# Performance work log

Measured on AMD Instinct MI355X. Metric: run time of the kernel, lower is better.

The kernel has to match this reference:

```python
import jax, jax.numpy as jnp
import numpy as np
import math

SIZE = 1024

def setup_inputs() -> dict:
    key = jax.random.key(0)
    k1, k2, k3, k4, k5 = jax.random.split(key, 5)
    B, Lq, Lc, D = 16, 2048, 2048, SIZE
    query = jax.random.normal(k1, (B, Lq, D), dtype=jnp.float32)
    bank = jax.random.normal(k2, (B, Lc, D), dtype=jnp.float32)
    # Linear weights stored torch-style as [out, in]; scaled like default init
    s = 1.0 / math.sqrt(D)
    Wc = jax.random.normal(k3, (D, D), dtype=jnp.float32) * s
    Woq = jax.random.normal(k4, (D, D), dtype=jnp.float32) * s
    Woc = jax.random.normal(k5, (D, D), dtype=jnp.float32) * s
    return {"query": query, "bank": bank, "Wc": Wc, "Woq": Woq, "Woc": Woc}

def reference(query, bank, Wc, Woq, Woc):
    # general attention: score = q @ (Wc bank)^T / sqrt(d)
    d = query.shape[-1]
    ctx_proj = jnp.einsum('bkd,ed->bke', bank, Wc)          # fc_context(bank)
    score = jnp.einsum('bqd,bkd->bqk', query, ctx_proj) / jnp.sqrt(jnp.float32(d))
    attn = jax.nn.softmax(score, axis=-1)                    # [B, Lq, Lc]
    context = jnp.einsum('bqk,bkd->bqd', attn, bank)
    output = jnp.einsum('bqd,ed->bqe', context, Woc) + jnp.einsum('bqd,ed->bqe', query, Woq)
    return (output, attn)
```

## Files before the change

### kernel.cpp

```cpp
#include <hip/hip_runtime.h>
#include <cstdint>

typedef unsigned short u16;
typedef __attribute__((ext_vector_type(8))) __bf16 bf16x8;
typedef __attribute__((ext_vector_type(4))) float f32x4;
typedef __attribute__((ext_vector_type(4))) unsigned short u16x4;

__device__ __forceinline__ u16 f2bf(float f) {
  unsigned u = __float_as_uint(f);
  u += 0x7fff + ((u >> 16) & 1);
  return (u16)(u >> 16);
}

__device__ __forceinline__ void g2l16(const void* g, void* l) {
  __builtin_amdgcn_global_load_lds(
      (const __attribute__((address_space(1))) unsigned int*)g,
      (__attribute__((address_space(3))) unsigned int*)l, 16, 0, 0);
}

template <int OUT_BF16>
__global__ void gemm_nt(const u16* __restrict__ A, const u16* __restrict__ B,
                        void* __restrict__ Cv,
                        int lda, int ldb, int ldc,
                        long sA, long sB, long sC,
                        int K, float scale)
{
  __shared__ char sm[16384];
  char* As = sm;
  char* Bs = sm + 8192;
  const int t = threadIdx.x;
  const int z = blockIdx.z;
  const u16* Ab = A + (long)z * sA + (long)(blockIdx.y * 128) * lda;
  const u16* Bb = B + (long)z * sB + (long)(blockIdx.x * 128) * ldb;

  const int wave = t >> 6, lane = t & 63;
  const int lm = lane & 15, quad = lane >> 4;
  const int wm = (wave >> 1) * 64, wn = (wave & 1) * 64;

  f32x4 acc[4][4] = {};

  const int sr = t >> 2;
  const int sc = (t & 3) * 8;
  const long aoff0 = (long)sr * lda + sc;
  const long aoff1 = (long)(sr + 64) * lda + sc;
  const long boff0 = (long)sr * ldb + sc;
  const long boff1 = (long)(sr + 64) * ldb + sc;
  char* lA0 = As + t * 16;  char* lA1 = As + 4096 + t * 16;
  char* lB0 = Bs + t * 16;  char* lB1 = Bs + 4096 + t * 16;

  for (int k0 = 0; k0 < K; k0 += 32) {
    __syncthreads();
    g2l16(Ab + aoff0 + k0, lA0);
    g2l16(Ab + aoff1 + k0, lA1);
    g2l16(Bb + boff0 + k0, lB0);
    g2l16(Bb + boff1 + k0, lB1);
    __syncthreads();

    bf16x8 af[4], bg[4];
#pragma unroll
    for (int i = 0; i < 4; ++i) {
      af[i] = *(const bf16x8*)(As + ((wm + i * 16 + lm) * 32 + quad * 8) * 2);
      bg[i] = *(const bf16x8*)(Bs + ((wn + i * 16 + lm) * 32 + quad * 8) * 2);
    }
#pragma unroll
    for (int i = 0; i < 4; ++i)
#pragma unroll
      for (int j = 0; j < 4; ++j)
        acc[i][j] = __builtin_amdgcn_mfma_f32_16x16x32_bf16(af[i], bg[j], acc[i][j], 0, 0, 0);
  }

  const int row0 = blockIdx.y * 128 + wm + quad * 4;
  const int col0 = blockIdx.x * 128 + wn + lm;
  if (OUT_BF16) {
    u16* C = (u16*)Cv + (long)z * sC;
#pragma unroll
    for (int i = 0; i < 4; ++i)
#pragma unroll
      for (int j = 0; j < 4; ++j)
#pragma unroll
        for (int r = 0; r < 4; ++r)
          C[(long)(row0 + i * 16 + r) * ldc + (col0 + j * 16)] = f2bf(acc[i][j][r] * scale);
  } else {
    float* C = (float*)Cv + (long)z * sC;
#pragma unroll
    for (int i = 0; i < 4; ++i)
#pragma unroll
      for (int j = 0; j < 4; ++j)
#pragma unroll
        for (int r = 0; r < 4; ++r)
          C[(long)(row0 + i * 16 + r) * ldc + (col0 + j * 16)] = acc[i][j][r] * scale;
  }
}

__global__ void softmax_rows(float* __restrict__ S, u16* __restrict__ P)
{
  const long row = blockIdx.x;
  float* p = S + row * 2048;
  u16*  q = P + row * 2048;
  const int t = threadIdx.x;
  float4 v0 = ((const float4*)p)[t];
  float4 v1 = ((const float4*)p)[t + 256];

  float m = fmaxf(fmaxf(fmaxf(v0.x, v0.y), fmaxf(v0.z, v0.w)),
                  fmaxf(fmaxf(v1.x, v1.y), fmaxf(v1.z, v1.w)));
#pragma unroll
  for (int s = 32; s; s >>= 1) m = fmaxf(m, __shfl_xor(m, s));
  __shared__ float red[4];
  if ((t & 63) == 0) red[t >> 6] = m;
  __syncthreads();
  m = fmaxf(fmaxf(red[0], red[1]), fmaxf(red[2], red[3]));

  v0.x = __expf(v0.x - m); v0.y = __expf(v0.y - m);
  v0.z = __expf(v0.z - m); v0.w = __expf(v0.w - m);
  v1.x = __expf(v1.x - m); v1.y = __expf(v1.y - m);
  v1.z = __expf(v1.z - m); v1.w = __expf(v1.w - m);

  float s8 = ((v0.x + v0.y) + (v0.z + v0.w)) + ((v1.x + v1.y) + (v1.z + v1.w));
#pragma unroll
  for (int s = 32; s; s >>= 1) s8 += __shfl_xor(s8, s);
  __syncthreads();
  if ((t & 63) == 0) red[t >> 6] = s8;
  __syncthreads();
  s8 = red[0] + red[1] + red[2] + red[3];
  const float inv = 1.0f / s8;

  v0.x *= inv; v0.y *= inv; v0.z *= inv; v0.w *= inv;
  v1.x *= inv; v1.y *= inv; v1.z *= inv; v1.w *= inv;
  ((float4*)p)[t] = v0;
  ((float4*)p)[t + 256] = v1;
  u16x4 b0 = { f2bf(v0.x), f2bf(v0.y), f2bf(v0.z), f2bf(v0.w) };
  u16x4 b1 = { f2bf(v1.x), f2bf(v1.y), f2bf(v1.z), f2bf(v1.w) };
  ((u16x4*)q)[t] = b0;
  ((u16x4*)q)[t + 256] = b1;
}

__global__ void transpose_cvt(const float* __restrict__ in, u16* __restrict__ out)
{
  __shared__ float tile[32][33];
  const int z = blockIdx.z;
  const float* ib = in + (long)z * 2048 * 1024;
  u16* ob = out + (long)z * 1024 * 2048;
  const int c0 = blockIdx.x * 32, r0 = blockIdx.y * 32;
  const int tx = threadIdx.x, ty = threadIdx.y;
#pragma unroll
  for (int k = 0; k < 32; k += 8)
    tile[ty + k][tx] = ib[(long)(r0 + ty + k) * 1024 + c0 + tx];
  __syncthreads();
#pragma unroll
  for (int k = 0; k < 32; k += 8)
    ob[(long)(c0 + ty + k) * 2048 + r0 + tx] = f2bf(tile[tx][ty + k]);
}

__global__ void cvt_bf16(const float* __restrict__ in, u16* __restrict__ out,
                         int ldo, long n)
{
  long i = ((long)blockIdx.x * 256 + threadIdx.x) * 4;
  if (i >= n) return;
  float4 v = *(const float4*)(in + i);
  long row = i >> 10;
  int col = (int)(i & 1023);
  u16x4 b = { f2bf(v.x), f2bf(v.y), f2bf(v.z), f2bf(v.w) };
  *(u16x4*)(out + row * (long)ldo + col) = b;
}

extern "C" void kernel_launch(void* const* d_in, const int* in_sizes, int n_in,
                              void* d_out, int out_size, void* d_ws, size_t ws_size,
                              hipStream_t stream)
{
  (void)in_sizes; (void)n_in; (void)out_size; (void)ws_size;
  const float* query = (const float*)d_in[0];
  const float* bank  = (const float*)d_in[1];
  const float* Wc    = (const float*)d_in[2];
  const float* Woq   = (const float*)d_in[3];
  const float* Woc   = (const float*)d_in[4];

  const long B = 16, L = 2048, D = 1024;
  float* out  = (float*)d_out;
  float* attn = out + B * L * D;

  u16* kb   = (u16*)d_ws;
  u16* cpb  = kb + B * L * D;
  u16* ab   = kb;
  u16* kbT  = cpb + B * L * D;
  u16* Acat = kbT + B * D * L;
  u16* Wcb  = Acat + B * L * 2048;
  u16* Wcat = Wcb + D * D;

  const long nQ = B * L * D;
  const long nW = D * D;

  cvt_bf16<<<dim3((unsigned)(nQ / 4 / 256)), 256, 0, stream>>>(bank, kb, 1024, nQ);
  cvt_bf16<<<dim3((unsigned)(nQ / 4 / 256)), 256, 0, stream>>>(query, Acat + 1024, 2048, nQ);
  cvt_bf16<<<dim3((unsigned)(nW / 4 / 256)), 256, 0, stream>>>(Wc, Wcb, 1024, nW);
  cvt_bf16<<<dim3((unsigned)(nW / 4 / 256)), 256, 0, stream>>>(Woc, Wcat, 2048, nW);
  cvt_bf16<<<dim3((unsigned)(nW / 4 / 256)), 256, 0, stream>>>(Woq, Wcat + 1024, 2048, nW);
  transpose_cvt<<<dim3(32, 64, 16), dim3(32, 8), 0, stream>>>(bank, kbT);

  gemm_nt<1><<<dim3(8, 16, 16), 256, 0, stream>>>(kb, Wcb, cpb,
      1024, 1024, 1024, L * D, 0, L * D, 1024, 1.0f);
  gemm_nt<0><<<dim3(16, 16, 16), 256, 0, stream>>>(Acat + 1024, cpb, attn,
      2048, 1024, 2048, L * 2048, L * D, L * 2048, 1024, 0.03125f);
  softmax_rows<<<dim3((unsigned)(B * L)), 256, 0, stream>>>(attn, ab);
  gemm_nt<1><<<dim3(8, 16, 16), 256, 0, stream>>>(ab, kbT, Acat,
      2048, 2048, 2048, L * 2048, D * 2048, L * 2048, 2048, 1.0f);
  gemm_nt<0><<<dim3(8, 16, 16), 256, 0, stream>>>(Acat, Wcat, out,
      2048, 2048, 1024, L * 2048, 0, L * D, 2048, 1.0f);
}
```

Baseline: 1.352 ms.

## Replace GEMM with 256x256 tiled, 4-stage LDS-pipelined 8-wave kernel

Replaces the single-buffered 128x128 GEMM with a 256x256-tile, 512-thread kernel. It uses a 4-deep ring of LDS buffers (128 KB dynamic shared memory) filled by async global-to-LDS loads, XOR-swizzled LDS addressing to avoid bank conflicts, and explicit vmcnt/barrier scheduling so loads overlap MFMA work. Block IDs are remapped for L2 locality, and MFMA sections raise wave priority. The aim is to remove the per-iteration load stalls and low arithmetic intensity of the old kernel. In exchange it uses much more LDS, which limits occupancy, and launches fewer blocks per GEMM.

```diff
diff --git a/kernel.cpp b/kernel.cpp
--- a/kernel.cpp
+++ b/kernel.cpp
@@ -18,63 +18,118 @@
       (__attribute__((address_space(3))) unsigned int*)l, 16, 0, 0);
 }
 
+__device__ __forceinline__ int swz(int q) { return q ^ (((q >> 7) & 7) << 4); }
+
 template <int OUT_BF16>
-__global__ void gemm_nt(const u16* __restrict__ A, const u16* __restrict__ B,
-                        void* __restrict__ Cv,
-                        int lda, int ldb, int ldc,
-                        long sA, long sB, long sC,
-                        int K, float scale)
-{
-  __shared__ char sm[16384];
-  char* As = sm;
-  char* Bs = sm + 8192;
+__global__ __launch_bounds__(512, 2)
+void gemm_nt_8p(const u16* __restrict__ A, const u16* __restrict__ B,
+                void* __restrict__ Cv,
+                int lda, int ldb, int ldc,
+                long sA, long sB, long sC,
+                int K, float scale)
+{
+  extern __shared__ char sm[];
   const int t = threadIdx.x;
+  const int lane = t & 63, wave = t >> 6;
+  const int lm = lane & 15, quad = lane >> 4;
+  const int wr = wave >> 2, wc = wave & 3;
+
+  const int gx = (int)gridDim.x;
+  const int npz = gx * (int)gridDim.y;
+  int lid = (int)blockIdx.x + gx * (int)blockIdx.y;
+  lid = (lid & 7) * (npz >> 3) + (lid >> 3);
+  const int bx = lid % gx, by = lid / gx;
   const int z = blockIdx.z;
-  const u16* Ab = A + (long)z * sA + (long)(blockIdx.y * 128) * lda;
-  const u16* Bb = B + (long)z * sB + (long)(blockIdx.x * 128) * ldb;
-
-  const int wave = t >> 6, lane = t & 63;
-  const int lm = lane & 15, quad = lane >> 4;
-  const int wm = (wave >> 1) * 64, wn = (wave & 1) * 64;
-
-  f32x4 acc[4][4] = {};
-
-  const int sr = t >> 2;
-  const int sc = (t & 3) * 8;
-  const long aoff0 = (long)sr * lda + sc;
-  const long aoff1 = (long)(sr + 64) * lda + sc;
-  const long boff0 = (long)sr * ldb + sc;
-  const long boff1 = (long)(sr + 64) * ldb + sc;
-  char* lA0 = As + t * 16;  char* lA1 = As + 4096 + t * 16;
-  char* lB0 = Bs + t * 16;  char* lB1 = Bs + 4096 + t * 16;
-
-  for (int k0 = 0; k0 < K; k0 += 32) {
-    __syncthreads();
-    g2l16(Ab + aoff0 + k0, lA0);
-    g2l16(Ab + aoff1 + k0, lA1);
-    g2l16(Bb + boff0 + k0, lB0);
-    g2l16(Bb + boff1 + k0, lB1);
-    __syncthreads();
-
-    bf16x8 af[4], bg[4];
-#pragma unroll
-    for (int i = 0; i < 4; ++i) {
-      af[i] = *(const bf16x8*)(As + ((wm + i * 16 + lm) * 32 + quad * 8) * 2);
-      bg[i] = *(const bf16x8*)(Bs + ((wn + i * 16 + lm) * 32 + quad * 8) * 2);
-    }
-#pragma unroll
-    for (int i = 0; i < 4; ++i)
-#pragma unroll
-      for (int j = 0; j < 4; ++j)
-        acc[i][j] = __builtin_amdgcn_mfma_f32_16x16x32_bf16(af[i], bg[j], acc[i][j], 0, 0, 0);
-  }
-
-  const int row0 = blockIdx.y * 128 + wm + quad * 4;
-  const int col0 = blockIdx.x * 128 + wn + lm;
+
+  const char* Ab = (const char*)(A + (long)z * sA + (long)(by * 256) * lda);
+  const char* Bb = (const char*)(B + (long)z * sB + (long)(bx * 256) * ldb);
+
+  const int q0 = t * 16;
+  const int ql = swz(q0);
+  const int srow = ql >> 6, scb = ql & 63;
+  const char* pA0 = Ab + (long)srow * (lda * 2) + scb;
+  const char* pA1 = pA0 + (long)128 * (lda * 2);
+  const char* pB0 = Bb + (long)srow * (ldb * 2) + scb;
+  const char* pB1 = pB0 + (long)128 * (ldb * 2);
+
+#define AOF(i) swz((wr * 128 + (i) * 16 + lm) * 64 + quad * 16)
+#define BOF(j) swz((wc * 64 + (j) * 16 + lm) * 64 + quad * 16)
+  const int aoff0 = AOF(0), aoff1 = AOF(1), aoff2 = AOF(2), aoff3 = AOF(3);
+  const int aoff4 = AOF(4), aoff5 = AOF(5), aoff6 = AOF(6), aoff7 = AOF(7);
+  const int boff0 = BOF(0), boff1 = BOF(1), boff2 = BOF(2), boff3 = BOF(3);
+
+  f32x4 acc[8][4] = {};
+  bf16x8 a0, a1, a2, a3, b0, b1, b2, b3;
+  const int NT = K >> 5;
+
+#define STAGE_A(tau) { char* d_ = sm + (((tau) & 3) << 14) + q0;              \
+    g2l16(pA0, d_); g2l16(pA1, d_ + 8192); pA0 += 64; pA1 += 64; }
+#define STAGE_B(tau) { char* d_ = sm + 65536 + (((tau) & 3) << 14) + q0;      \
+    g2l16(pB0, d_); g2l16(pB1, d_ + 8192); pB0 += 64; pB1 += 64; }
+
+#define MFMA4(I, AR)                                                          \
+  acc[I][0] = __builtin_amdgcn_mfma_f32_16x16x32_bf16(AR, b0, acc[I][0], 0, 0, 0); \
+  acc[I][1] = __builtin_amdgcn_mfma_f32_16x16x32_bf16(AR, b1, acc[I][1], 0, 0, 0); \
+  acc[I][2] = __builtin_amdgcn_mfma_f32_16x16x32_bf16(AR, b2, acc[I][2], 0, 0, 0); \
+  acc[I][3] = __builtin_amdgcn_mfma_f32_16x16x32_bf16(AR, b3, acc[I][3], 0, 0, 0);
+
+#define PHASE_A(tau, DO_STAGE) {                                              \
+    char* Abuf_ = sm + (((tau) & 3) << 14);                                   \
+    char* Bbuf_ = Abuf_ + 65536;                                              \
+    a0 = *(const bf16x8*)(Abuf_ + aoff0);                                     \
+    a1 = *(const bf16x8*)(Abuf_ + aoff1);                                     \
+    a2 = *(const bf16x8*)(Abuf_ + aoff2);                                     \
+    a3 = *(const bf16x8*)(Abuf_ + aoff3);                                     \
+    b0 = *(const bf16x8*)(Bbuf_ + boff0);                                     \
+    b1 = *(const bf16x8*)(Bbuf_ + boff1);                                     \
+    b2 = *(const bf16x8*)(Bbuf_ + boff2);                                     \
+    b3 = *(const bf16x8*)(Bbuf_ + boff3);                                     \
+    if (DO_STAGE) STAGE_A((tau) + 3)                                          \
+    __builtin_amdgcn_s_barrier();                                             \
+    asm volatile("s_waitcnt lgkmcnt(0)" ::: "memory");                        \
+    __builtin_amdgcn_s_setprio(1);                                            \
+    MFMA4(0, a0) MFMA4(1, a1) MFMA4(2, a2) MFMA4(3, a3)                       \
+    __builtin_amdgcn_s_setprio(0);                                            \
+    __builtin_amdgcn_s_barrier();                                             \
+  }
+
+#define PHASE_B(tau, DO_STAGE, VM, ENDBAR) {                                  \
+    char* Abuf_ = sm + (((tau) & 3) << 14);                                   \
+    a0 = *(const bf16x8*)(Abuf_ + aoff4);                                     \
+    a1 = *(const bf16x8*)(Abuf_ + aoff5);                                     \
+    a2 = *(const bf16x8*)(Abuf_ + aoff6);                                     \
+    a3 = *(const bf16x8*)(Abuf_ + aoff7);                                     \
+    if (DO_STAGE) STAGE_B((tau) + 3)                                          \
+    __builtin_amdgcn_s_barrier();                                             \
+    asm volatile("s_waitcnt lgkmcnt(0)" ::: "memory");                        \
+    __builtin_amdgcn_s_setprio(1);                                            \
+    MFMA4(4, a0) MFMA4(5, a1) MFMA4(6, a2) MFMA4(7, a3)                       \
+    __builtin_amdgcn_s_setprio(0);                                            \
+    asm volatile(VM ::: "memory");                                            \
+    if (ENDBAR) __builtin_amdgcn_s_barrier();                                 \
+  }
+
+  STAGE_A(0) STAGE_B(0) STAGE_A(1) STAGE_B(1) STAGE_A(2) STAGE_B(2)
+  asm volatile("s_waitcnt vmcnt(8)" ::: "memory");
+  __builtin_amdgcn_s_barrier();
+
+  for (int tau = 0; tau < NT - 3; ++tau) {
+    PHASE_A(tau, 1)
+    PHASE_B(tau, 1, "s_waitcnt vmcnt(8)", 1)
+  }
+  PHASE_A(NT - 3, 0)
+  PHASE_B(NT - 3, 0, "s_waitcnt vmcnt(4)", 1)
+  PHASE_A(NT - 2, 0)
+  PHASE_B(NT - 2, 0, "s_waitcnt vmcnt(0)", 1)
+  PHASE_A(NT - 1, 0)
+  PHASE_B(NT - 1, 0, "", 0)
+
+  const int row0 = by * 256 + wr * 128 + quad * 4;
+  const int col0 = bx * 256 + wc * 64 + lm;
   if (OUT_BF16) {
     u16* C = (u16*)Cv + (long)z * sC;
 #pragma unroll
-    for (int i = 0; i < 4; ++i)
+    for (int i = 0; i < 8; ++i)
 #pragma unroll
       for (int j = 0; j < 4; ++j)
 #pragma unroll
@@ -83,7 +138,7 @@
   } else {
     float* C = (float*)Cv + (long)z * sC;
 #pragma unroll
-    for (int i = 0; i < 4; ++i)
+    for (int i = 0; i < 8; ++i)
 #pragma unroll
       for (int j = 0; j < 4; ++j)
 #pragma unroll
@@ -189,6 +244,11 @@
   const long nQ = B * L * D;
   const long nW = D * D;
 
+  hipFuncSetAttribute(reinterpret_cast<const void*>(gemm_nt_8p<1>),
+                      hipFuncAttributeMaxDynamicSharedMemorySize, 131072);
+  hipFuncSetAttribute(reinterpret_cast<const void*>(gemm_nt_8p<0>),
+                      hipFuncAttributeMaxDynamicSharedMemorySize, 131072);
+
   cvt_bf16<<<dim3((unsigned)(nQ / 4 / 256)), 256, 0, stream>>>(bank, kb, 1024, nQ);
   cvt_bf16<<<dim3((unsigned)(nQ / 4 / 256)), 256, 0, stream>>>(query, Acat + 1024, 2048, nQ);
   cvt_bf16<<<dim3((unsigned)(nW / 4 / 256)), 256, 0, stream>>>(Wc, Wcb, 1024, nW);
@@ -196,13 +256,13 @@
   cvt_bf16<<<dim3((unsigned)(nW / 4 / 256)), 256, 0, stream>>>(Woq, Wcat + 1024, 2048, nW);
   transpose_cvt<<<dim3(32, 64, 16), dim3(32, 8), 0, stream>>>(bank, kbT);
 
-  gemm_nt<1><<<dim3(8, 16, 16), 256, 0, stream>>>(kb, Wcb, cpb,
+  gemm_nt_8p<1><<<dim3(4, 8, 16), 512, 131072, stream>>>(kb, Wcb, cpb,
       1024, 1024, 1024, L * D, 0, L * D, 1024, 1.0f);
-  gemm_nt<0><<<dim3(16, 16, 16), 256, 0, stream>>>(Acat + 1024, cpb, attn,
+  gemm_nt_8p<0><<<dim3(8, 8, 16), 512, 131072, stream>>>(Acat + 1024, cpb, attn,
       2048, 1024, 2048, L * 2048, L * D, L * 2048, 1024, 0.03125f);
   softmax_rows<<<dim3((unsigned)(B * L)), 256, 0, stream>>>(attn, ab);
-  gemm_nt<1><<<dim3(8, 16, 16), 256, 0, stream>>>(ab, kbT, Acat,
+  gemm_nt_8p<1><<<dim3(4, 8, 16), 512, 131072, stream>>>(ab, kbT, Acat,
       2048, 2048, 2048, L * 2048, D * 2048, L * 2048, 2048, 1.0f);
-  gemm_nt<0><<<dim3(8, 16, 16), 256, 0, stream>>>(Acat, Wcat, out,
+  gemm_nt_8p<0><<<dim3(4, 8, 16), 512, 131072, stream>>>(Acat, Wcat, out,
       2048, 2048, 1024, L * 2048, 0, L * D, 2048, 1.0f);
 }
```

New measurement: 1.211 ms. 1.12x faster.
